# Kernel optimization log

Hardware: AMD Instinct MI355X
Metric: run time of the kernel (lower is better)

The kernel has to match this reference:

```python
import jax, jax.numpy as jnp
import numpy as np

B, T, D = 2, 2048, 2048
H, DK = 16, 96
DV = 192                 # head_v_dim = head_dim * expand_v (expand_v=2)
KEY_DIM = H * DK         # 1536 = 0.75*D
VAL_DIM = H * DV         # 3072 = 1.5*D
KS = 4                   # short-conv kernel size
EPS = 1e-6


def setup_inputs() -> dict:
    key = jax.random.key(0)
    ks = jax.random.split(key, 16)
    nrm = lambda k, shape, s: jax.random.normal(k, shape, jnp.float32) * s
    # dt_bias init as in the torch module
    dt_min, dt_max = 1e-3, 1e-1
    dt = jnp.exp(jax.random.uniform(ks[12], (H,), jnp.float32)
                 * (np.log(dt_max) - np.log(dt_min)) + np.log(dt_min))
    dt_bias = dt + jnp.log(-jnp.expm1(-dt))
    return {
        'x': nrm(ks[0], (B, T, D), 1.0),
        'Wq': nrm(ks[1], (D, KEY_DIM), D ** -0.5),
        'Wk': nrm(ks[2], (D, KEY_DIM), D ** -0.5),
        'Wv': nrm(ks[3], (D, VAL_DIM), D ** -0.5),
        'Wb': nrm(ks[4], (D, H), D ** -0.5),
        'Wa': nrm(ks[5], (D, H), D ** -0.5),
        'Wg': nrm(ks[6], (D, VAL_DIM), D ** -0.5),
        'Wo': nrm(ks[7], (VAL_DIM, D), VAL_DIM ** -0.5),
        'conv_q_w': nrm(ks[8], (KEY_DIM, KS), KS ** -0.5),
        'conv_k_w': nrm(ks[9], (KEY_DIM, KS), KS ** -0.5),
        'conv_v_w': nrm(ks[10], (VAL_DIM, KS), KS ** -0.5),
        'A_log': jnp.log(jax.random.uniform(ks[11], (H,), jnp.float32, 1e-4, 16.0)),
        'dt_bias': dt_bias,
        'o_norm_weight': jnp.ones((DV,), jnp.float32),
    }


def _causal_depthwise_conv(x, w):
    # x: (B, T, C), w: (C, KS). Depthwise causal conv + SiLU.
    xp = jnp.pad(x, ((0, 0), (KS - 1, 0), (0, 0)))
    y = sum(xp[:, j:j + T, :] * w[:, j] for j in range(KS))
    return jax.nn.silu(y)


def _gated_delta_scan(q, k, v, g, beta):
    # q,k: (B,T,H,DK)  v: (B,T,H,DV)  g,beta: (B,T,H)
    def step(S, inp):
        q_t, k_t, v_t, g_t, b_t = inp          # (B,H,DK),(B,H,DK),(B,H,DV),(B,H),(B,H)
        alpha = jnp.exp(g_t)                   # (B,H)
        retrieved = jnp.einsum('bhk,bhkv->bhv', k_t, S)
        error = v_t - retrieved                # (B,H,DV)
        S = alpha[:, :, None, None] * S + b_t[:, :, None, None] * (
            k_t[:, :, :, None] * error[:, :, None, :])
        o_t = jnp.einsum('bhk,bhkv->bhv', q_t, S)
        return S, o_t

    tm = lambda a: jnp.swapaxes(a, 0, 1)       # time-major
    S0 = jnp.zeros((B, H, DK, DV), jnp.float32)
    _, o = jax.lax.scan(step, S0, (tm(q), tm(k), tm(v), tm(g), tm(beta)))
    return jnp.swapaxes(o, 0, 1)               # (B,T,H,DV)


def reference(x, Wq, Wk, Wv, Wb, Wa, Wg, Wo,
              conv_q_w, conv_k_w, conv_v_w, A_log, dt_bias, o_norm_weight):
    # projections + causal depthwise short conv + SiLU
    q = _causal_depthwise_conv(x @ Wq, conv_q_w).reshape(B, T, H, DK)
    k = _causal_depthwise_conv(x @ Wk, conv_k_w).reshape(B, T, H, DK)
    v = _causal_depthwise_conv(x @ Wv, conv_v_w).reshape(B, T, H, DV)

    beta = jax.nn.sigmoid(x @ Wb)                                   # (B,T,H)
    g = -jnp.exp(A_log) * jax.nn.softplus(x @ Wa + dt_bias)         # (B,T,H)

    # qk L2 normalization (use_qk_l2norm_in_kernel=True path)
    q = q * jax.lax.rsqrt(jnp.sum(q * q, -1, keepdims=True) + 1e-12)
    k = k * jax.lax.rsqrt(jnp.sum(k * k, -1, keepdims=True) + 1e-12)

    o = _gated_delta_scan(q, k, v, g, beta)                         # (B,T,H,DV)

    # gated RMSNorm over head_v_dim
    g_out = (x @ Wg).reshape(B, T, H, DV)
    rms = jax.lax.rsqrt(jnp.mean(o * o, -1, keepdims=True) + EPS)
    o = (o * rms) * o_norm_weight * jax.nn.sigmoid(g_out)

    return o.reshape(B, T, VAL_DIM) @ Wo                            # (B,T,D)
```

## Files before the change

kernel.cpp:

```cpp
#include <hip/hip_runtime.h>

#define B_ 2
#define T_ 2048
#define D_ 2048
#define H_ 16
#define DK_ 96
#define DV_ 192
#define KEYD 1536
#define VALD 3072
#define NPROJ 9216
#define PQK 6144
#define KS_ 4
#define C_ 64
#define NC_ 32

typedef unsigned short u16;
typedef unsigned int u32;
typedef __bf16 bf16x8 __attribute__((ext_vector_type(8)));
typedef float f32x4 __attribute__((ext_vector_type(4)));

__device__ __forceinline__ u16 f2bf(float f) {
  unsigned u = __float_as_uint(f);
  u += 0x7FFF + ((u >> 16) & 1);
  return (u16)(u >> 16);
}
__device__ __forceinline__ float bf2f(u16 v) { return __uint_as_float((unsigned)v << 16); }
__device__ __forceinline__ float bflo(u32 w) { return __uint_as_float(w << 16); }
__device__ __forceinline__ float bfhi(u32 w) { return __uint_as_float(w & 0xFFFF0000u); }

__device__ __forceinline__ void gll16(const void* g, void* lds) {
  __builtin_amdgcn_global_load_lds(
      (const __attribute__((address_space(1))) void*)g,
      (__attribute__((address_space(3))) void*)lds, 16, 0, 0);
}

__global__ __launch_bounds__(256) void cast_x(const float* __restrict__ in,
                                              u16* __restrict__ out, int n4) {
  int i = blockIdx.x * 256 + threadIdx.x;
  if (i < n4) {
    float4 v = reinterpret_cast<const float4*>(in)[i];
    ushort4 o;
    o.x = f2bf(v.x); o.y = f2bf(v.y); o.z = f2bf(v.z); o.w = f2bf(v.w);
    reinterpret_cast<ushort4*>(out)[i] = o;
  }
}

__global__ __launch_bounds__(256) void transpose_cast(const float* __restrict__ src,
                                                      u16* __restrict__ dst, int R, int C) {
  __shared__ float tile[32][33];
  int tx = threadIdx.x & 31, ty = threadIdx.x >> 5;
  int c0 = blockIdx.x * 32, r0 = blockIdx.y * 32;
#pragma unroll
  for (int j = 0; j < 4; ++j)
    tile[ty + j * 8][tx] = src[(size_t)(r0 + ty + j * 8) * C + c0 + tx];
  __syncthreads();
#pragma unroll
  for (int j = 0; j < 4; ++j)
    dst[(size_t)(c0 + ty + j * 8) * R + r0 + tx] = f2bf(tile[tx][ty + j * 8]);
}

template <int OUT16>
__global__ __launch_bounds__(512, 2) void gemm256(const u16* __restrict__ A,
    const u16* __restrict__ BT, u16* __restrict__ C0, u16* __restrict__ C1,
    float* __restrict__ Cf, int M, int N, int K, int nsplit, int s0, int s1) {
  __shared__ u16 LA[2][256 * 64];
  __shared__ u16 LB[2][256 * 64];
  const int tid = threadIdx.x, wave = tid >> 6, lane = tid & 63;
  const int l15 = lane & 15, l16 = lane >> 4, x7 = l15 & 7;
  const int wr = wave >> 2, wc = wave & 3;
  const int m0 = blockIdx.y * 256, n0 = blockIdx.x * 256;
  const int r8 = lane >> 3;
  const int csrc = ((lane & 7) ^ r8) << 3;
  const int NKT = K >> 6;
  f32x4 acc[8][4] = {};

#define STAGE(p, kt) { \
    const u16* As_ = A + (size_t)m0 * K + (size_t)(kt) * 64; \
    const u16* Bs_ = BT + (size_t)n0 * K + (size_t)(kt) * 64; \
    _Pragma("unroll") \
    for (int j = 0; j < 4; ++j) { \
      int rowb = j * 64 + wave * 8; \
      gll16(As_ + (size_t)(rowb + r8) * K + csrc, (char*)&LA[p][0] + rowb * 128); \
      gll16(Bs_ + (size_t)(rowb + r8) * K + csrc, (char*)&LB[p][0] + rowb * 128); \
    } \
  }

#define LDA8(p, mh, dst) { \
    _Pragma("unroll") \
    for (int mi = 0; mi < 4; ++mi) \
      _Pragma("unroll") \
      for (int kk = 0; kk < 2; ++kk) { \
        int row = wr * 128 + (mh) * 64 + mi * 16 + l15; \
        dst[mi * 2 + kk] = *(const bf16x8*)((const char*)&LA[p][0] + row * 128 + (((kk * 4 + l16) ^ x7) << 4)); \
      } \
  }

#define LDB4(p, nh, dst) { \
    _Pragma("unroll") \
    for (int ni = 0; ni < 2; ++ni) \
      _Pragma("unroll") \
      for (int kk = 0; kk < 2; ++kk) { \
        int row = wc * 64 + (nh) * 32 + ni * 16 + l15; \
        dst[ni * 2 + kk] = *(const bf16x8*)((const char*)&LB[p][0] + row * 128 + (((kk * 4 + l16) ^ x7) << 4)); \
      } \
  }

#define MMQ(AF, BF, mbase, nbase) { \
    __builtin_amdgcn_s_setprio(1); \
    _Pragma("unroll") \
    for (int mi = 0; mi < 4; ++mi) \
      _Pragma("unroll") \
      for (int ni = 0; ni < 2; ++ni) \
        _Pragma("unroll") \
        for (int kk = 0; kk < 2; ++kk) \
          acc[(mbase) + mi][(nbase) + ni] = __builtin_amdgcn_mfma_f32_16x16x32_bf16( \
              AF[mi * 2 + kk], BF[ni * 2 + kk], acc[(mbase) + mi][(nbase) + ni], 0, 0, 0); \
    __builtin_amdgcn_s_setprio(0); \
  }

#define BAR() { __builtin_amdgcn_s_barrier(); asm volatile("" ::: "memory"); }

  STAGE(0, 0);
  if (NKT > 1) {
    STAGE(1, 1);
    asm volatile("s_waitcnt vmcnt(8)" ::: "memory");
  } else {
    asm volatile("s_waitcnt vmcnt(0)" ::: "memory");
  }
  BAR();

  bf16x8 afA[8], afB[8], bf0[4], bf1[4];
  LDA8(0, 0, afA); LDB4(0, 0, bf0);

  for (int c = 0; c < NKT; ++c) {
    int p = c & 1;
    LDB4(p, 1, bf1);
    BAR();
    MMQ(afA, bf0, 0, 0);
    LDA8(p, 1, afB);
    BAR();
    MMQ(afA, bf1, 0, 2);
    BAR();
    MMQ(afB, bf0, 4, 0);
    if (c + 2 < NKT) {
      STAGE(p, c + 2);
      asm volatile("s_waitcnt vmcnt(8)" ::: "memory");
    } else if (c + 1 < NKT) {
      asm volatile("s_waitcnt vmcnt(0)" ::: "memory");
    }
    BAR();
    if (c + 1 < NKT) { LDA8(p ^ 1, 0, afA); LDB4(p ^ 1, 0, bf0); }
    MMQ(afB, bf1, 4, 2);
  }

#pragma unroll
  for (int mi = 0; mi < 8; ++mi)
#pragma unroll
    for (int ni = 0; ni < 4; ++ni)
#pragma unroll
      for (int j = 0; j < 4; ++j) {
        int row = m0 + wr * 128 + mi * 16 + l16 * 4 + j;
        int col = n0 + wc * 64 + ni * 16 + l15;
        float v = acc[mi][ni][j];
        if (OUT16) {
          if (col < nsplit) C0[(size_t)row * s0 + col] = f2bf(v);
          else              C1[(size_t)row * s1 + col - nsplit] = f2bf(v);
        } else {
          Cf[(size_t)row * N + col] = v;
        }
      }
#undef STAGE
#undef LDA8
#undef LDB4
#undef MMQ
#undef BAR
}

template <int OUT16>
__global__ __launch_bounds__(256) void gemm_bt(const u16* __restrict__ A,
                                               const u16* __restrict__ BT,
                                               u16* __restrict__ C0, u16* __restrict__ C1,
                                               float* __restrict__ Cf,
                                               int M, int N, int K, int nsplit, int s0, int s1) {
  __shared__ u16 As[128 * 32];
  __shared__ u16 Bs[128 * 32];
  int tid = threadIdx.x;
  int wave = tid >> 6, lane = tid & 63;
  int l15 = lane & 15, l16 = lane >> 4;
  int m0 = blockIdx.y * 128, n0 = blockIdx.x * 128;
  int wm = (wave >> 1) * 64, wn = (wave & 1) * 64;
  f32x4 acc[4][4] = {};
  int nkt = K >> 5;
  for (int kt = 0; kt < nkt; ++kt) {
    int k0 = kt << 5;
    __syncthreads();
#pragma unroll
    for (int rr = 0; rr < 2; ++rr) {
      int idx = tid + rr * 256;
      int row = idx >> 2, kc8 = (idx & 3) * 8;
      unsigned loff = (unsigned)(rr * 256 + wave * 64) * 16;
      gll16(A + (size_t)(m0 + row) * K + k0 + kc8, (char*)As + loff);
      gll16(BT + (size_t)(n0 + row) * K + k0 + kc8, (char*)Bs + loff);
    }
    __syncthreads();
    bf16x8 af[4], bfr[4];
#pragma unroll
    for (int i = 0; i < 4; ++i)
      af[i] = *reinterpret_cast<const bf16x8*>(&As[(wm + i * 16 + l15) * 32 + l16 * 8]);
#pragma unroll
    for (int i = 0; i < 4; ++i)
      bfr[i] = *reinterpret_cast<const bf16x8*>(&Bs[(wn + i * 16 + l15) * 32 + l16 * 8]);
#pragma unroll
    for (int mi = 0; mi < 4; ++mi)
#pragma unroll
      for (int ni = 0; ni < 4; ++ni)
        acc[mi][ni] = __builtin_amdgcn_mfma_f32_16x16x32_bf16(af[mi], bfr[ni], acc[mi][ni], 0, 0, 0);
  }
#pragma unroll
  for (int mi = 0; mi < 4; ++mi)
#pragma unroll
    for (int ni = 0; ni < 4; ++ni)
#pragma unroll
      for (int j = 0; j < 4; ++j) {
        int row = m0 + wm + mi * 16 + l16 * 4 + j;
        int col = n0 + wn + ni * 16 + l15;
        if (OUT16) {
          if (col < nsplit) C0[(size_t)row * s0 + col] = f2bf(acc[mi][ni][j]);
          else              C1[(size_t)row * s1 + col - nsplit] = f2bf(acc[mi][ni][j]);
        } else {
          Cf[(size_t)row * N + col] = acc[mi][ni][j];
        }
      }
}

__global__ __launch_bounds__(256) void proj_bg(const float* __restrict__ x,
    const float* __restrict__ Wb, const float* __restrict__ Wa,
    const float* __restrict__ A_log, const float* __restrict__ dt_bias,
    float* __restrict__ beta, float* __restrict__ gg) {
  __shared__ float xs[4 * 2048];
  __shared__ float red[4][32][8];
  int tid = threadIdx.x;
  int r0 = blockIdx.x * 4;
  for (int i = tid; i < 4 * 2048; i += 256)
    xs[i] = x[(size_t)r0 * D_ + i];
  __syncthreads();
  int colg = tid & 31, ks = tid >> 5;
  const float* W = (colg < 16) ? Wb : Wa;
  int wc = colg & 15;
  float p0 = 0, p1 = 0, p2 = 0, p3 = 0;
  int kbeg = ks * 256;
  for (int k = kbeg; k < kbeg + 256; ++k) {
    float wv = W[k * H_ + wc];
    p0 += xs[k] * wv;
    p1 += xs[2048 + k] * wv;
    p2 += xs[4096 + k] * wv;
    p3 += xs[6144 + k] * wv;
  }
  red[0][colg][ks] = p0; red[1][colg][ks] = p1;
  red[2][colg][ks] = p2; red[3][colg][ks] = p3;
  __syncthreads();
  if (tid < 128) {
    int row = tid >> 5, col = tid & 31;
    float d = 0;
#pragma unroll
    for (int i = 0; i < 8; ++i) d += red[row][col][i];
    int r = r0 + row;
    if (col < 16) {
      beta[(size_t)r * H_ + col] = 1.f / (1.f + __expf(-d));
    } else {
      int hh = col - 16;
      float z = d + dt_bias[hh];
      float sp = (z > 20.f) ? z : log1pf(__expf(z));
      gg[(size_t)r * H_ + hh] = -__expf(A_log[hh]) * sp;
    }
  }
}

__global__ __launch_bounds__(256) void conv_qkv(const u16* __restrict__ Pqkv,
    const float* __restrict__ wq, const float* __restrict__ wk, const float* __restrict__ wv,
    u16* __restrict__ qc, u16* __restrict__ kc, u16* __restrict__ vc) {
  int bt = blockIdx.x;
  int t = bt & (T_ - 1);
  int tid = threadIdx.x, h = tid >> 4, li = tid & 15;
#pragma unroll
  for (int part = 0; part < 2; ++part) {
    const float* w = part ? wk : wq;
    const u16* base = Pqkv + (size_t)bt * PQK + part * KEYD + h * DK_;
    float y[6]; float ss = 0.f;
#pragma unroll
    for (int jj = 0; jj < 6; ++jj) {
      int c = li + jj * 16;
      int ch = h * DK_ + c;
      float a = 0.f;
#pragma unroll
      for (int j = 0; j < KS_; ++j) {
        int dt = j - (KS_ - 1);
        if (t + dt >= 0) a += bf2f(base[(ptrdiff_t)dt * PQK + c]) * w[ch * KS_ + j];
      }
      float yv = a / (1.f + __expf(-a));
      y[jj] = yv; ss += yv * yv;
    }
    ss += __shfl_xor(ss, 1); ss += __shfl_xor(ss, 2);
    ss += __shfl_xor(ss, 4); ss += __shfl_xor(ss, 8);
    float rn = rsqrtf(ss + 1e-12f);
    u16* out = (part ? kc : qc) + (size_t)bt * KEYD + h * DK_;
#pragma unroll
    for (int jj = 0; jj < 6; ++jj) out[li + jj * 16] = f2bf(y[jj] * rn);
  }
  const u16* vbase = Pqkv + (size_t)bt * PQK + 2 * KEYD;
  u16* vout = vc + (size_t)bt * VALD;
#pragma unroll
  for (int jj = 0; jj < 12; ++jj) {
    int c = tid + jj * 256;
    float a = 0.f;
#pragma unroll
    for (int j = 0; j < KS_; ++j) {
      int dt = j - (KS_ - 1);
      if (t + dt >= 0) a += bf2f(vbase[(ptrdiff_t)dt * PQK + c]) * wv[c * KS_ + j];
    }
    vout[c] = f2bf(a / (1.f + __expf(-a)));
  }
}

__global__ __launch_bounds__(320) void chunk_prep(
    const u16* __restrict__ kc, u16* __restrict__ Uv ,
    const float* __restrict__ gg, const float* __restrict__ beta,
    u16* __restrict__ Wg, float* __restrict__ Gcum,
    float* __restrict__ cdArr, float* __restrict__ lamArr) {
  __shared__ __align__(16) u16 ktL[64 * 104];
  __shared__ float AmL[64 * 68];
  __shared__ float glL[64], GclL[64], blL[64], DplL[64];
  int tid = threadIdx.x;
  int flat = blockIdx.x;
  int c = flat & 31, bh = flat >> 5, h = bh & 15, b = bh >> 4;
  int bT0 = b * T_ + c * 64;

  {
    const u32* kg = (const u32*)(kc + (size_t)bT0 * KEYD + h * DK_);
    for (int i = tid; i < 3072; i += 320) {
      int t = i / 48, dd = i - t * 48;
      ((u32*)ktL)[t * 52 + dd] = kg[(size_t)t * (KEYD / 2) + dd];
    }
  }
  if (tid < 64) {
    float g = gg[(size_t)(bT0 + tid) * H_ + h];
    float bv = beta[(size_t)(bT0 + tid) * H_ + h];
    float v = g;
#pragma unroll
    for (int off = 1; off < 64; off <<= 1) {
      float u = __shfl_up(v, off);
      if (tid >= off) v += u;
    }
    float g63 = __shfl(v, 63);
    glL[tid] = g; GclL[tid] = v; blL[tid] = bv; DplL[tid] = __expf(v - g);
    Gcum[(size_t)flat * 64 + tid] = v;
    cdArr[(size_t)flat * 64 + tid] = bv * __expf(g63 - v);
    if (tid == 63) lamArr[flat] = __expf(v);
  }
  __syncthreads();

  {
    int wave = tid >> 6, lane = tid & 63, l15 = lane & 15, l16 = lane >> 4;
    if (wave < 4) {
      f32x4 ac[4] = {};
#pragma unroll
      for (int ks = 0; ks < 3; ++ks) {
        bf16x8 a = *(const bf16x8*)&ktL[(wave * 16 + l15) * 104 + ks * 32 + l16 * 8];
#pragma unroll
        for (int n = 0; n < 4; ++n) {
          bf16x8 bb = *(const bf16x8*)&ktL[(n * 16 + l15) * 104 + ks * 32 + l16 * 8];
          ac[n] = __builtin_amdgcn_mfma_f32_16x16x32_bf16(a, bb, ac[n], 0, 0, 0);
        }
      }
#pragma unroll
      for (int n = 0; n < 4; ++n)
#pragma unroll
        for (int j = 0; j < 4; ++j) {
          int t = wave * 16 + l16 * 4 + j;
          int jj = n * 16 + l15;
          float val = 0.f;
          if (jj < t) val = __expf((GclL[t] - glL[t]) - GclL[jj]) * blL[jj] * ac[n][j];
          AmL[t * 68 + jj] = val;
        }
    }
  }
  __syncthreads();

  if (tid < 288) {
    int j = tid;
    float m[64];
    if (j < 192) {
      const u16* up = Uv + (size_t)bT0 * VALD + h * DV_ + j;
#pragma unroll
      for (int t = 0; t < 64; ++t) m[t] = bf2f(up[(size_t)t * VALD]);
    } else {
      int d = j - 192;
#pragma unroll
      for (int t = 0; t < 64; ++t) m[t] = DplL[t] * bf2f(ktL[t * 104 + d]);
    }
#pragma unroll
    for (int t0 = 0; t0 < 64; t0 += 4) {
      {
        f32x4 a1 = *(const f32x4*)&AmL[(t0 + 1) * 68 + t0];
        m[t0 + 1] -= a1[0] * m[t0];
        f32x4 a2 = *(const f32x4*)&AmL[(t0 + 2) * 68 + t0];
        m[t0 + 2] -= a2[0] * m[t0] + a2[1] * m[t0 + 1];
        f32x4 a3 = *(const f32x4*)&AmL[(t0 + 3) * 68 + t0];
        m[t0 + 3] -= a3[0] * m[t0] + a3[1] * m[t0 + 1] + a3[2] * m[t0 + 2];
      }
#pragma unroll
      for (int tp = t0 + 4; tp < 64; ++tp) {
        f32x4 a = *(const f32x4*)&AmL[tp * 68 + t0];
        m[tp] -= a[0] * m[t0] + a[1] * m[t0 + 1] + a[2] * m[t0 + 2] + a[3] * m[t0 + 3];
      }
    }
    if (j < 192) {
      u16* up = Uv + (size_t)bT0 * VALD + h * DV_ + j;
#pragma unroll
      for (int t = 0; t < 64; ++t) up[(size_t)t * VALD] = f2bf(m[t]);
    } else {
      int d = j - 192;
      u16* wp = Wg + (size_t)bT0 * KEYD + h * DK_ + d;
#pragma unroll
      for (int t = 0; t < 64; ++t) wp[(size_t)t * KEYD] = f2bf(m[t]);
    }
  }
}

__global__ __launch_bounds__(256) void serial_state(
    const u16* __restrict__ kc, const u16* __restrict__ Wg, u16* __restrict__ Ue,
    const float* __restrict__ cdArr, const float* __restrict__ lamArr,
    u16* __restrict__ Schk) {
  __shared__ __align__(16) u16 WtL[2][64 * 104];
  __shared__ __align__(16) u16 ktT[2][96 * 72];
  __shared__ __align__(16) u16 StH[32 * 104];
  __shared__ __align__(16) u16 StLo[32 * 104];
  __shared__ __align__(16) u16 EtH[32 * 72];
  __shared__ __align__(16) u16 EtLo[32 * 72];
  __shared__ float lamS[2];

  int tid = threadIdx.x, wave = tid >> 6, lane = tid & 63;
  int l15 = lane & 15, l16 = lane >> 4;
  int jq = blockIdx.x % 6, bh = blockIdx.x / 6, h = bh & 15, b = bh >> 4;
  int col0 = jq * 32;
  int ntS = wave & 1, m3 = 3 * (wave >> 1);
  int st_t = tid >> 2, st_dd = (tid & 3) * 12;

  f32x4 Sf[3] = {};
  uint4 wreg[3], kreg[3];
  u16 ureg[2][4];
  float cdv[4];
  float lamReg;

#define PREFETCH(bT0p, flatp) { \
    const u32* wgp = (const u32*)(Wg + (size_t)((bT0p) + st_t) * KEYD + h * DK_) + st_dd; \
    const u32* kgp = (const u32*)(kc + (size_t)((bT0p) + st_t) * KEYD + h * DK_) + st_dd; \
    wreg[0] = ((const uint4*)wgp)[0]; wreg[1] = ((const uint4*)wgp)[1]; wreg[2] = ((const uint4*)wgp)[2]; \
    kreg[0] = ((const uint4*)kgp)[0]; kreg[1] = ((const uint4*)kgp)[1]; kreg[2] = ((const uint4*)kgp)[2]; \
    _Pragma("unroll") \
    for (int ni = 0; ni < 2; ++ni) \
      _Pragma("unroll") \
      for (int j = 0; j < 4; ++j) \
        ureg[ni][j] = Ue[(size_t)((bT0p) + wave * 16 + l16 * 4 + j) * VALD + h * DV_ + col0 + ni * 16 + l15]; \
    _Pragma("unroll") \
    for (int j = 0; j < 4; ++j) cdv[j] = cdArr[(size_t)(flatp) * 64 + wave * 16 + l16 * 4 + j]; \
    if (tid == 0) lamReg = lamArr[flatp]; \
  }

  PREFETCH(b * T_, bh * NC_);

  for (int c = 0; c < NC_; ++c) {
    int buf = c & 1;
    int flat = bh * NC_ + c;
    int bT0 = b * T_ + (c << 6);
    {
      u32* wl = (u32*)&WtL[buf][0] + st_t * 52 + st_dd;
      ((uint4*)wl)[0] = wreg[0];
      *(uint4*)(wl + 4) = wreg[1];
      *(uint4*)(wl + 8) = wreg[2];
#pragma unroll
      for (int r = 0; r < 3; ++r) {
        u32 vals[4] = {kreg[r].x, kreg[r].y, kreg[r].z, kreg[r].w};
#pragma unroll
        for (int e = 0; e < 4; ++e) {
          int d = 2 * (st_dd + r * 4 + e);
          ktT[buf][d * 72 + st_t] = (u16)(vals[e] & 0xFFFFu);
          ktT[buf][(d + 1) * 72 + st_t] = (u16)(vals[e] >> 16);
        }
      }
      int cl = ntS * 16 + l15;
      u16* schkRow = Schk + (size_t)flat * (DK_ * DV_) + (size_t)(col0 + cl) * DK_;
#pragma unroll
      for (int i = 0; i < 3; ++i) {
        u16 hi0 = f2bf(Sf[i][0]), hi1 = f2bf(Sf[i][1]);
        u16 hi2 = f2bf(Sf[i][2]), hi3 = f2bf(Sf[i][3]);
        int dbase = (m3 + i) * 16 + l16 * 4;
        StH[cl * 104 + dbase + 0] = hi0; StLo[cl * 104 + dbase + 0] = f2bf(Sf[i][0] - bf2f(hi0));
        StH[cl * 104 + dbase + 1] = hi1; StLo[cl * 104 + dbase + 1] = f2bf(Sf[i][1] - bf2f(hi1));
        StH[cl * 104 + dbase + 2] = hi2; StLo[cl * 104 + dbase + 2] = f2bf(Sf[i][2] - bf2f(hi2));
        StH[cl * 104 + dbase + 3] = hi3; StLo[cl * 104 + dbase + 3] = f2bf(Sf[i][3] - bf2f(hi3));
        u32* ow = (u32*)(schkRow + dbase);
        ow[0] = ((u32)hi1 << 16) | hi0;
        ow[1] = ((u32)hi3 << 16) | hi2;
      }
      if (tid == 0) lamS[buf] = lamReg;
    }
    __syncthreads();
    {
      f32x4 Ea[2] = {};
#pragma unroll
      for (int ks = 0; ks < 3; ++ks) {
        bf16x8 a = *(const bf16x8*)&WtL[buf][(wave * 16 + l15) * 104 + ks * 32 + l16 * 8];
#pragma unroll
        for (int ni = 0; ni < 2; ++ni) {
          bf16x8 bhv = *(const bf16x8*)&StH[(ni * 16 + l15) * 104 + ks * 32 + l16 * 8];
          bf16x8 blv = *(const bf16x8*)&StLo[(ni * 16 + l15) * 104 + ks * 32 + l16 * 8];
          Ea[ni] = __builtin_amdgcn_mfma_f32_16x16x32_bf16(a, bhv, Ea[ni], 0, 0, 0);
          Ea[ni] = __builtin_amdgcn_mfma_f32_16x16x32_bf16(a, blv, Ea[ni], 0, 0, 0);
        }
      }
#pragma unroll
      for (int ni = 0; ni < 2; ++ni)
#pragma unroll
        for (int j = 0; j < 4; ++j) {
          int t = wave * 16 + l16 * 4 + j;
          float ev = bf2f(ureg[ni][j]) - Ea[ni][j];
          Ue[(size_t)(bT0 + t) * VALD + h * DV_ + col0 + ni * 16 + l15] = f2bf(ev);
          float ep = cdv[j] * ev;
          u16 ehi = f2bf(ep);
          int cl = ni * 16 + l15;
          EtH[cl * 72 + t] = ehi;
          EtLo[cl * 72 + t] = f2bf(ep - bf2f(ehi));
        }
      if (c + 1 < NC_) PREFETCH(bT0 + 64, flat + 1);
    }
    __syncthreads();
    {
      float lam = lamS[buf];
#pragma unroll
      for (int i = 0; i < 3; ++i)
#pragma unroll
        for (int j = 0; j < 4; ++j) Sf[i][j] *= lam;
#pragma unroll
      for (int ks = 0; ks < 2; ++ks) {
        bf16x8 bhv = *(const bf16x8*)&EtH[(ntS * 16 + l15) * 72 + ks * 32 + l16 * 8];
        bf16x8 blv = *(const bf16x8*)&EtLo[(ntS * 16 + l15) * 72 + ks * 32 + l16 * 8];
#pragma unroll
        for (int i = 0; i < 3; ++i) {
          bf16x8 a = *(const bf16x8*)&ktT[buf][((m3 + i) * 16 + l15) * 72 + ks * 32 + l16 * 8];
          Sf[i] = __builtin_amdgcn_mfma_f32_16x16x32_bf16(a, bhv, Sf[i], 0, 0, 0);
          Sf[i] = __builtin_amdgcn_mfma_f32_16x16x32_bf16(a, blv, Sf[i], 0, 0, 0);
        }
      }
    }
  }
#undef PREFETCH
}

__global__ __launch_bounds__(256) void chunk_out(
    const u16* __restrict__ qc, const u16* __restrict__ kc, const u16* __restrict__ Ee,
    const u16* __restrict__ Schk, const float* __restrict__ Gcum,
    const float* __restrict__ beta, u16* __restrict__ osc) {
  __shared__ __align__(16) char pool[65280];
  u16* qL   = (u16*)pool;
  u16* BmL  = (u16*)(pool + 12288);
  u16* BmLo = (u16*)(pool + 21504);
  u16* kL   = (u16*)(pool + 30720);
  u16* StL  = (u16*)(pool + 30720);
  u16* EtL  = (u16*)(pool + 50688);
  float* GclL = (float*)(pool + 64512);
  float* blL  = (float*)(pool + 64768);
  float* DlL  = (float*)(pool + 65024);

  int tid = threadIdx.x, wave = tid >> 6, lane = tid & 63;
  int l15 = lane & 15, l16 = lane >> 4;
  int flat = blockIdx.x;
  int c = flat & 31, bh = flat >> 5, h = bh & 15, b = bh >> 4;
  int bT0 = b * T_ + c * 64;

  {
    const u32* qg = (const u32*)(qc + (size_t)bT0 * KEYD + h * DK_);
    const u32* kg = (const u32*)(kc + (size_t)bT0 * KEYD + h * DK_);
    for (int i = tid; i < 3072; i += 256) {
      int t = i / 48, dd = i - t * 48;
      ((u32*)qL)[t * 48 + dd] = qg[(size_t)t * (KEYD / 2) + dd];
      ((u32*)kL)[t * 48 + dd] = kg[(size_t)t * (KEYD / 2) + dd];
    }
    if (tid < 64) {
      float gv = Gcum[(size_t)flat * 64 + tid];
      GclL[tid] = gv;
      DlL[tid] = __expf(gv);
      blL[tid] = beta[(size_t)(bT0 + tid) * H_ + h];
    }
  }
  __syncthreads();

  {
    f32x4 bacc[4] = {};
#pragma unroll
    for (int kk = 0; kk < 3; ++kk) {
      bf16x8 aq = *(const bf16x8*)&qL[(wave * 16 + l15) * 96 + kk * 32 + l16 * 8];
#pragma unroll
      for (int n = 0; n < 4; ++n) {
        bf16x8 bk = *(const bf16x8*)&kL[(n * 16 + l15) * 96 + kk * 32 + l16 * 8];
        bacc[n] = __builtin_amdgcn_mfma_f32_16x16x32_bf16(aq, bk, bacc[n], 0, 0, 0);
      }
    }
#pragma unroll
    for (int n = 0; n < 4; ++n)
#pragma unroll
      for (int j = 0; j < 4; ++j) {
        int t = wave * 16 + l16 * 4 + j;
        int jj = n * 16 + l15;
        float val = 0.f;
        if (jj <= t) val = __expf(GclL[t] - GclL[jj]) * blL[jj] * bacc[n][j];
        u16 hi = f2bf(val);
        BmL[t * 72 + jj] = hi;
        BmLo[t * 72 + jj] = f2bf(val - bf2f(hi));
      }
  }
  __syncthreads();

#pragma unroll
  for (int half = 0; half < 2; ++half) {
    {
      const u32* sg = (const u32*)(Schk + (size_t)flat * (DK_ * DV_) + (size_t)(half * 96) * DK_);
      for (int i = tid; i < 4608; i += 256) {
        int cL = i / 48, dd = i - cL * 48;
        ((u32*)&StL[cL * 104])[dd] = sg[cL * 48 + dd];
      }
      const u32* eg = (const u32*)(Ee + (size_t)bT0 * VALD + h * DV_ + half * 96);
      for (int i = tid; i < 3072; i += 256) {
        int t = i / 48, dd = i - t * 48;
        u32 w2 = eg[(size_t)t * (VALD / 2) + dd];
        EtL[(2 * dd) * 72 + t]     = (u16)(w2 & 0xFFFF);
        EtL[(2 * dd + 1) * 72 + t] = (u16)(w2 >> 16);
      }
    }
    __syncthreads();
    f32x4 oacc[6] = {};
#pragma unroll
    for (int kk = 0; kk < 3; ++kk) {
      bf16x8 aq = *(const bf16x8*)&qL[(wave * 16 + l15) * 96 + kk * 32 + l16 * 8];
#pragma unroll
      for (int n = 0; n < 6; ++n) {
        bf16x8 bs = *(const bf16x8*)&StL[(n * 16 + l15) * 104 + kk * 32 + l16 * 8];
        oacc[n] = __builtin_amdgcn_mfma_f32_16x16x32_bf16(aq, bs, oacc[n], 0, 0, 0);
      }
    }
#pragma unroll
    for (int n = 0; n < 6; ++n)
#pragma unroll
      for (int j = 0; j < 4; ++j)
        oacc[n][j] *= DlL[wave * 16 + l16 * 4 + j];
#pragma unroll
    for (int kk = 0; kk < 2; ++kk) {
      bf16x8 ah = *(const bf16x8*)&BmL[(wave * 16 + l15) * 72 + kk * 32 + l16 * 8];
      bf16x8 al = *(const bf16x8*)&BmLo[(wave * 16 + l15) * 72 + kk * 32 + l16 * 8];
#pragma unroll
      for (int n = 0; n < 6; ++n) {
        bf16x8 be = *(const bf16x8*)&EtL[(n * 16 + l15) * 72 + kk * 32 + l16 * 8];
        oacc[n] = __builtin_amdgcn_mfma_f32_16x16x32_bf16(ah, be, oacc[n], 0, 0, 0);
        oacc[n] = __builtin_amdgcn_mfma_f32_16x16x32_bf16(al, be, oacc[n], 0, 0, 0);
      }
    }
#pragma unroll
    for (int n = 0; n < 6; ++n)
#pragma unroll
      for (int j = 0; j < 4; ++j) {
        int t = wave * 16 + l16 * 4 + j;
        int cc = half * 96 + n * 16 + l15;
        osc[(size_t)(bT0 + t) * VALD + h * DV_ + cc] = f2bf(oacc[n][j]);
      }
    __syncthreads();
  }
}

__global__ __launch_bounds__(256) void rmsnorm_gate(const u16* __restrict__ o,
    const u16* __restrict__ Pg, const float* __restrict__ w, u16* __restrict__ onb) {
  int bt = blockIdx.x;
  int tid = threadIdx.x, h = tid >> 4, li = tid & 15;
  const u16* orow = o + (size_t)bt * VALD + h * DV_;
  const u16* grow = Pg + (size_t)bt * VALD + h * DV_;
  float y[12]; float ss = 0.f;
#pragma unroll
  for (int jj = 0; jj < 12; ++jj) {
    float v = bf2f(orow[li + jj * 16]);
    y[jj] = v; ss += v * v;
  }
  ss += __shfl_xor(ss, 1); ss += __shfl_xor(ss, 2);
  ss += __shfl_xor(ss, 4); ss += __shfl_xor(ss, 8);
  float rms = rsqrtf(ss * (1.f / DV_) + 1e-6f);
  u16* out = onb + (size_t)bt * VALD + h * DV_;
#pragma unroll
  for (int jj = 0; jj < 12; ++jj) {
    int c = li + jj * 16;
    float gv = bf2f(grow[c]);
    float sig = 1.f / (1.f + __expf(-gv));
    out[c] = f2bf(y[jj] * rms * w[c] * sig);
  }
}

extern "C" void kernel_launch(void* const* d_in, const int* in_sizes, int n_in,
                              void* d_out, int out_size, void* d_ws, size_t ws_size,
                              hipStream_t stream) {
  (void)in_sizes; (void)n_in; (void)out_size; (void)ws_size;
  const float* x      = (const float*)d_in[0];
  const float* Wq     = (const float*)d_in[1];
  const float* Wk     = (const float*)d_in[2];
  const float* Wv     = (const float*)d_in[3];
  const float* Wb     = (const float*)d_in[4];
  const float* Wa     = (const float*)d_in[5];
  const float* Wg     = (const float*)d_in[6];
  const float* Wo     = (const float*)d_in[7];
  const float* cqw    = (const float*)d_in[8];
  const float* ckw    = (const float*)d_in[9];
  const float* cvw    = (const float*)d_in[10];
  const float* A_log  = (const float*)d_in[11];
  const float* dt_bias= (const float*)d_in[12];
  const float* onw    = (const float*)d_in[13];
  float* out = (float*)d_out;

  char* ws = (char*)d_ws;
  u16*   xb    = (u16*)  (ws + 0);
  u16*   WT    = (u16*)  (ws + 16777216);
  u16*   qc    = (u16*)  (ws + 0);
  u16*   kc    = (u16*)  (ws + 12582912);
  u16*   vc    = (u16*)  (ws + 25165824);
  u16*   Pqkv  = (u16*)  (ws + 54525952);
  u16*   Wbuf  = (u16*)  (ws + 54525952);
  u16*   Schk  = (u16*)  (ws + 67108864);
  u16*   Pg    = (u16*)  (ws + 104857600);
  u16*   osc   = (u16*)  (ws + 130023424);
  float* beta  = (float*)(ws + 155189248);
  float* gg    = (float*)(ws + 155451392);
  float* Gcum  = (float*)(ws + 155713536);
  float* cdArr = (float*)(ws + 155975680);
  float* lamArr= (float*)(ws + 156237824);
  u16*   onb   = (u16*)  (ws + 54525952);
  u16*   WoT   = (u16*)  (ws + 79691776);

  int n4 = B_ * T_ * D_ / 4;
  cast_x<<<(n4 + 255) / 256, 256, 0, stream>>>(x, xb, n4);
  transpose_cast<<<dim3(48, 64), 256, 0, stream>>>(Wq, WT, 2048, 1536);
  transpose_cast<<<dim3(48, 64), 256, 0, stream>>>(Wk, WT + (size_t)1536 * 2048, 2048, 1536);
  transpose_cast<<<dim3(96, 64), 256, 0, stream>>>(Wv, WT + (size_t)3072 * 2048, 2048, 3072);
  transpose_cast<<<dim3(96, 64), 256, 0, stream>>>(Wg, WT + (size_t)6144 * 2048, 2048, 3072);

  gemm256<1><<<dim3(NPROJ / 256, (B_ * T_) / 256), 512, 0, stream>>>(
      xb, WT, Pqkv, Pg, nullptr, B_ * T_, NPROJ, D_, PQK, PQK, VALD);
  proj_bg<<<(B_ * T_) / 4, 256, 0, stream>>>(x, Wb, Wa, A_log, dt_bias, beta, gg);
  conv_qkv<<<B_ * T_, 256, 0, stream>>>(Pqkv, cqw, ckw, cvw, qc, kc, vc);

  chunk_prep<<<B_ * H_ * NC_, 320, 0, stream>>>(kc, vc, gg, beta, Wbuf, Gcum, cdArr, lamArr);
  serial_state<<<B_ * H_ * 6, 256, 0, stream>>>(kc, Wbuf, vc, cdArr, lamArr, Schk);
  chunk_out<<<B_ * H_ * NC_, 256, 0, stream>>>(qc, kc, vc, Schk, Gcum, beta, osc);

  rmsnorm_gate<<<B_ * T_, 256, 0, stream>>>(osc, Pg, onw, onb);
  transpose_cast<<<dim3(64, 96), 256, 0, stream>>>(Wo, WoT, 3072, 2048);
  gemm_bt<0><<<dim3(D_ / 128, (B_ * T_) / 128), 256, 0, stream>>>(
      onb, WoT, nullptr, nullptr, out, B_ * T_, D_, VALD, 0, 0, 0);
}
```

Before: 649.0 us.

## Interleave split global-to-LDS staging with MFMA quadrants in gemm256

The 256x256 GEMM main loop is re-scheduled. The single bulk STAGE of the next-next K tile is split into A-half and B pieces, and each piece is issued between the four MFMA quadrants. LDS fragment reads now happen at the start of each iteration, with explicit lgkmcnt(0) waits and sched_barriers, instead of being prefetched across iterations. The aim is to spread global-load issue evenly over the compute so memory and MFMA overlap better. In exchange, the loop carries more barriers per iteration and loses the cross-iteration register prefetch of the first fragments.

```diff
diff --git a/kernel.cpp b/kernel.cpp
--- a/kernel.cpp
+++ b/kernel.cpp
@@ -74,13 +74,19 @@
   const int NKT = K >> 6;
   f32x4 acc[8][4] = {};
 
-#define STAGE(p, kt) { \
+#define STG_A(p, kt, half) { \
     const u16* As_ = A + (size_t)m0 * K + (size_t)(kt) * 64; \
+    _Pragma("unroll") \
+    for (int g = 0; g < 2; ++g) { \
+      int rowb = g * 128 + (half) * 64 + wave * 8; \
+      gll16(As_ + (size_t)(rowb + r8) * K + csrc, (char*)&LA[p][0] + rowb * 128); \
+    } \
+  }
+#define STG_B(p, kt) { \
     const u16* Bs_ = BT + (size_t)n0 * K + (size_t)(kt) * 64; \
     _Pragma("unroll") \
     for (int j = 0; j < 4; ++j) { \
       int rowb = j * 64 + wave * 8; \
-      gll16(As_ + (size_t)(rowb + r8) * K + csrc, (char*)&LA[p][0] + rowb * 128); \
       gll16(Bs_ + (size_t)(rowb + r8) * K + csrc, (char*)&LB[p][0] + rowb * 128); \
     } \
   }
@@ -94,7 +100,6 @@
         dst[mi * 2 + kk] = *(const bf16x8*)((const char*)&LA[p][0] + row * 128 + (((kk * 4 + l16) ^ x7) << 4)); \
       } \
   }
-
 #define LDB4(p, nh, dst) { \
     _Pragma("unroll") \
     for (int ni = 0; ni < 2; ++ni) \
@@ -118,39 +123,48 @@
     __builtin_amdgcn_s_setprio(0); \
   }
 
-#define BAR() { __builtin_amdgcn_s_barrier(); asm volatile("" ::: "memory"); }
-
-  STAGE(0, 0);
+#define BARR() __builtin_amdgcn_s_barrier()
+#define LGKM0() { asm volatile("s_waitcnt lgkmcnt(0)" ::: "memory"); __builtin_amdgcn_sched_barrier(0); }
+
+  STG_A(0, 0, 0); STG_A(0, 0, 1); STG_B(0, 0);
   if (NKT > 1) {
-    STAGE(1, 1);
+    STG_A(1, 1, 0); STG_A(1, 1, 1); STG_B(1, 1);
     asm volatile("s_waitcnt vmcnt(8)" ::: "memory");
   } else {
     asm volatile("s_waitcnt vmcnt(0)" ::: "memory");
   }
-  BAR();
+  BARR();
 
   bf16x8 afA[8], afB[8], bf0[4], bf1[4];
-  LDA8(0, 0, afA); LDB4(0, 0, bf0);
-
   for (int c = 0; c < NKT; ++c) {
-    int p = c & 1;
+    const int p = c & 1;
+    const bool stg = (c + 2 < NKT);
+    LDA8(p, 0, afA); LDB4(p, 0, bf0);
+    BARR();
+    LGKM0();
+    MMQ(afA, bf0, 0, 0);
+    BARR();
     LDB4(p, 1, bf1);
-    BAR();
-    MMQ(afA, bf0, 0, 0);
+    if (stg) STG_A(p, c + 2, 0);
+    BARR();
+    LGKM0();
+    MMQ(afA, bf1, 0, 2);
+    BARR();
     LDA8(p, 1, afB);
-    BAR();
-    MMQ(afA, bf1, 0, 2);
-    BAR();
-    MMQ(afB, bf0, 4, 0);
-    if (c + 2 < NKT) {
-      STAGE(p, c + 2);
+    if (stg) STG_B(p, c + 2);
+    BARR();
+    LGKM0();
+    MMQ(afB, bf1, 4, 2);
+    BARR();
+    if (stg) {
+      STG_A(p, c + 2, 1);
       asm volatile("s_waitcnt vmcnt(8)" ::: "memory");
     } else if (c + 1 < NKT) {
       asm volatile("s_waitcnt vmcnt(0)" ::: "memory");
     }
-    BAR();
-    if (c + 1 < NKT) { LDA8(p ^ 1, 0, afA); LDB4(p ^ 1, 0, bf0); }
-    MMQ(afB, bf1, 4, 2);
+    BARR();
+    MMQ(afB, bf0, 4, 0);
+    BARR();
   }
 
 #pragma unroll
@@ -169,11 +183,13 @@
           Cf[(size_t)row * N + col] = v;
         }
       }
-#undef STAGE
+#undef STG_A
+#undef STG_B
 #undef LDA8
 #undef LDB4
 #undef MMQ
-#undef BAR
+#undef BARR
+#undef LGKM0
 }
 
 template <int OUT16>
```

Result: faster. 631.3 us (-2.7%).
